# Performance work log

Measured on AMD Instinct MI355X. Metric: run time of the kernel, lower is better.

## Reference

```python
import jax, jax.numpy as jnp
import numpy as np

B, C, D, H = 2, 1024, 1024, 16
DH = D // H
EPS = 1e-8


def setup_inputs() -> dict:
    key = jax.random.key(0)
    ks = jax.random.split(key, 12)
    s = 0.02
    return {
        "x": jax.random.normal(ks[0], (B, C, D), dtype=jnp.float32),
        "rms_w": jnp.ones((C, D), dtype=jnp.float32),
        "rms_b": jnp.zeros((C, D), dtype=jnp.float32),
        "Wqkv": jax.random.normal(ks[1], (3 * D, D), dtype=jnp.float32) * s,
        "Wout": jax.random.normal(ks[2], (D, D), dtype=jnp.float32) * s,
        "bout": jnp.zeros((D,), dtype=jnp.float32),
        "Wf": jax.random.normal(ks[3], (D, D), dtype=jnp.float32) * s,
        "bf": jnp.zeros((D,), dtype=jnp.float32),
        "Ww": jax.random.normal(ks[4], (D, D), dtype=jnp.float32) * s,
        "bw": jnp.zeros((D,), dtype=jnp.float32),
        "Wv": jax.random.normal(ks[5], (D, D), dtype=jnp.float32) * s,
        "bv": jnp.zeros((D,), dtype=jnp.float32),
        "beta": jnp.ones((1,), dtype=jnp.float32),
    }


def _rope_cos_sin(C, dh):
    # faithful to source: theta = 10000 ** (-2*(i-1)/dh), i in [0, dh//2)
    i = jnp.arange(dh // 2, dtype=jnp.float32)
    theta = 10000.0 ** (-2.0 * (i - 1.0) / dh)            # [dh//2]
    ang = jnp.arange(C, dtype=jnp.float32)[:, None] * theta  # [C, dh//2]
    return jnp.cos(ang), jnp.sin(ang)


def _rotate(t, cos, sin):
    # equivalent to einsum('bhci,cij->bhcj', t, R) with the source R
    ev, od = t[..., 0::2], t[..., 1::2]          # [B,H,C,dh//2]
    out_ev = ev * cos + od * sin
    out_od = -ev * sin + od * cos
    return jnp.stack([out_ev, out_od], axis=-1).reshape(t.shape)


def _rmsnorm(x, w, b):
    rms = jnp.sqrt(jnp.mean(x * x, axis=-1, keepdims=True) + EPS)
    return w * (x / rms) + b


def _attention(x, Wqkv, Wout, bout):
    qkv = x @ Wqkv.T                               # [B,C,3D]
    q, k, v = jnp.split(qkv, 3, axis=-1)
    def heads(t):
        return t.reshape(B, C, H, DH).transpose(0, 2, 1, 3)  # [B,H,C,dh]
    q, k, v = heads(q), heads(k), heads(v)
    cos, sin = _rope_cos_sin(C, DH)
    qr = _rotate(q, cos, sin)
    kr = _rotate(k, cos, sin)
    scale = 1.0 / jnp.sqrt(jnp.float32(DH))
    num = jnp.exp(jnp.einsum('bhid,bhjd->bhij', qr, kr) * scale)
    den = jnp.sum(jnp.exp(jnp.einsum('bhid,bhjd->bhij', q, k) * scale),
                  axis=-1, keepdims=True)
    attn = num / den
    mask = jnp.tril(jnp.ones((C, C), dtype=bool))
    attn = jnp.where(mask[None, None], attn, 0.0)
    y = attn @ v                                   # [B,H,C,dh]
    y = y.transpose(0, 2, 1, 3).reshape(B, C, D)
    return y @ Wout.T + bout


def _ffn(x, Wf, bf, Ww, bw, Wv, bv, beta):
    h = x @ Wf.T + bf
    wx = h @ Ww.T + bw
    swish = wx * jax.nn.sigmoid(beta * wx)
    return swish * (h @ Wv.T + bv)


def reference(x, rms_w, rms_b, Wqkv, Wout, bout, Wf, bf, Ww, bw, Wv, bv, beta):
    # dropout p is identity in eval mode
    x = _rmsnorm(x, rms_w, rms_b)
    x = x + _attention(x, Wqkv, Wout, bout)
    x = _rmsnorm(x, rms_w, rms_b)   # same shared RMSNorm module applied twice
    x = x + _ffn(x, Wf, bf, Ww, bw, Wv, bv, beta)
    return x
```

## Files before the change

### kernel.cpp

```cpp
#include <hip/hip_runtime.h>
#include <math.h>

#define B_ 2
#define C_ 1024
#define D_ 1024
#define H_ 16
#define DH_ 64
#define EPSF 1e-8f
#define BK 32

typedef __bf16 bf16;
typedef __attribute__((ext_vector_type(4))) __bf16 bf16x4;
typedef __attribute__((ext_vector_type(8))) __bf16 bf16x8;
typedef __attribute__((ext_vector_type(4))) float f32x4;

__device__ inline f32x4 mfma16(bf16x8 a, bf16x8 b, f32x4 c) {
  return __builtin_amdgcn_mfma_f32_16x16x32_bf16(a, b, c, 0, 0, 0);
}

__device__ inline void async16(const bf16* g, bf16* l) {
  __builtin_amdgcn_global_load_lds((const __attribute__((address_space(1))) void*)g,
                                   (__attribute__((address_space(3))) void*)l, 16, 0, 0);
}

__device__ inline float rope_theta(float i) {
  return exp2f(-13.287712379549449f * (2.0f * (i - 1.0f) * (1.0f / 64.0f)));
}

__global__ __launch_bounds__(256) void cvt_rms_kernel(const float* __restrict__ wqkv,
                                                      const float* __restrict__ wout,
                                                      const float* __restrict__ wf,
                                                      const float* __restrict__ www,
                                                      const float* __restrict__ wv,
                                                      bf16* __restrict__ wdst,
                                                      const float* __restrict__ x,
                                                      const float* __restrict__ rw,
                                                      const float* __restrict__ rb,
                                                      bf16* __restrict__ xout) {
  __shared__ float red[4];
  int t = threadIdx.x;
  if (blockIdx.x < 7 * 1024) {
    int seg = blockIdx.x >> 10;
    int local = (blockIdx.x & 1023) * 1024 + t * 4;
    const float* src = seg < 3 ? wqkv + (size_t)seg * (D_ * D_)
                     : seg == 3 ? wout : seg == 4 ? wf : seg == 5 ? www : wv;
    float4 v = *(const float4*)(src + local);
    bf16x4 o;
    o[0] = (bf16)v.x; o[1] = (bf16)v.y; o[2] = (bf16)v.z; o[3] = (bf16)v.w;
    *(bf16x4*)(wdst + (size_t)seg * (D_ * D_) + local) = o;
    return;
  }
  int row = blockIdx.x - 7 * 1024;
  int c = row & (C_ - 1);
  float4 xv = *(const float4*)(x + (size_t)row * D_ + t * 4);
  float ss = xv.x * xv.x + xv.y * xv.y + xv.z * xv.z + xv.w * xv.w;
#pragma unroll
  for (int m = 1; m < 64; m <<= 1) ss += __shfl_xor(ss, m, 64);
  if ((t & 63) == 0) red[t >> 6] = ss;
  __syncthreads();
  float tot = red[0] + red[1] + red[2] + red[3];
  float inv = rsqrtf(tot * (1.0f / D_) + EPSF);
  float4 wv4 = *(const float4*)(rw + (size_t)c * D_ + t * 4);
  float4 bv4 = *(const float4*)(rb + (size_t)c * D_ + t * 4);
  bf16x4 ov;
  ov[0] = (bf16)(wv4.x * (xv.x * inv) + bv4.x);
  ov[1] = (bf16)(wv4.y * (xv.y * inv) + bv4.y);
  ov[2] = (bf16)(wv4.z * (xv.z * inv) + bv4.z);
  ov[3] = (bf16)(wv4.w * (xv.w * inv) + bv4.w);
  *(bf16x4*)(xout + (size_t)row * D_ + t * 4) = ov;
}

__global__ __launch_bounds__(256) void rmsnorm_bf16_kernel(const bf16* __restrict__ x,
                                                           const float* __restrict__ w,
                                                           const float* __restrict__ b,
                                                           bf16* __restrict__ out) {
  int row = blockIdx.x;
  int c = row & (C_ - 1);
  int t = threadIdx.x;
  bf16x4 xv = *(const bf16x4*)(x + (size_t)row * D_ + t * 4);
  float f0 = (float)xv[0], f1 = (float)xv[1], f2 = (float)xv[2], f3 = (float)xv[3];
  float ss = f0 * f0 + f1 * f1 + f2 * f2 + f3 * f3;
#pragma unroll
  for (int m = 1; m < 64; m <<= 1) ss += __shfl_xor(ss, m, 64);
  __shared__ float red[4];
  if ((t & 63) == 0) red[t >> 6] = ss;
  __syncthreads();
  float tot = red[0] + red[1] + red[2] + red[3];
  float inv = rsqrtf(tot * (1.0f / D_) + EPSF);
  float4 wv = *(const float4*)(w + (size_t)c * D_ + t * 4);
  float4 bv = *(const float4*)(b + (size_t)c * D_ + t * 4);
  bf16x4 ov;
  ov[0] = (bf16)(wv.x * (f0 * inv) + bv.x);
  ov[1] = (bf16)(wv.y * (f1 * inv) + bv.y);
  ov[2] = (bf16)(wv.z * (f2 * inv) + bv.z);
  ov[3] = (bf16)(wv.w * (f3 * inv) + bv.w);
  *(bf16x4*)(out + (size_t)row * D_ + t * 4) = ov;
}

template <int BMt, int BNt>
__global__ __launch_bounds__(256) void gemm_lds(const bf16* __restrict__ A,
                                                const bf16* __restrict__ W,
                                                const float* __restrict__ bias,
                                                const bf16* __restrict__ R,
                                                bf16* __restrict__ Cout,
                                                int M, int N, int K) {
  constexpr int MT = BMt / 32;
  constexpr int NT = BNt / 32;
  __shared__ bf16 sa[BMt * BK];
  __shared__ bf16 sb[BNt * BK];
  int t = threadIdx.x, l = t & 63, w = t >> 6;
  int m0 = blockIdx.y * BMt;
  int n0 = blockIdx.x * BNt;
  int wm = (w >> 1) * (BMt / 2), wn = (w & 1) * (BNt / 2);
  int lm = l & 15, lq = l >> 4;
  f32x4 acc[MT][NT] = {};

  for (int k0 = 0; k0 < K; k0 += BK) {
    __syncthreads();
#pragma unroll
    for (int p = 0; p < BMt / 64; ++p) {
      int lin = p * 256 + t;
      async16(A + (size_t)(m0 + (lin >> 2)) * K + k0 + (lin & 3) * 8, sa + lin * 8);
    }
#pragma unroll
    for (int p = 0; p < BNt / 64; ++p) {
      int lin = p * 256 + t;
      async16(W + (size_t)(n0 + (lin >> 2)) * K + k0 + (lin & 3) * 8, sb + lin * 8);
    }
    __syncthreads();
    bf16x8 af[MT], bfr[NT];
#pragma unroll
    for (int mt = 0; mt < MT; ++mt)
      af[mt] = *(const bf16x8*)(sa + (wm + mt * 16 + lm) * BK + lq * 8);
#pragma unroll
    for (int nt = 0; nt < NT; ++nt)
      bfr[nt] = *(const bf16x8*)(sb + (wn + nt * 16 + lm) * BK + lq * 8);
#pragma unroll
    for (int mt = 0; mt < MT; ++mt)
#pragma unroll
      for (int nt = 0; nt < NT; ++nt)
        acc[mt][nt] = mfma16(af[mt], bfr[nt], acc[mt][nt]);
  }
#pragma unroll
  for (int mt = 0; mt < MT; ++mt)
#pragma unroll
    for (int nt = 0; nt < NT; ++nt) {
      int col = n0 + wn + nt * 16 + lm;
      float bb = bias ? bias[col] : 0.0f;
#pragma unroll
      for (int r = 0; r < 4; ++r) {
        int row = m0 + wm + mt * 16 + lq * 4 + r;
        float v = acc[mt][nt][r] + bb;
        if (R) v += (float)R[(size_t)row * N + col];
        Cout[(size_t)row * N + col] = (bf16)v;
      }
    }
}

__global__ __launch_bounds__(256) void gemm_qkv_kernel(const bf16* __restrict__ A,
                                                       const bf16* __restrict__ W,
                                                       bf16* __restrict__ qkv,
                                                       bf16* __restrict__ vt) {
  constexpr int BMt = 128, BNt = 64, MT = 4, NT = 2;
  const int N = 3 * D_, K = D_;
  __shared__ bf16 sa[BMt * BK];
  __shared__ bf16 sb[BNt * BK];
  __shared__ bf16 tv[64 * 136];
  int t = threadIdx.x, l = t & 63, w = t >> 6;
  int m0 = blockIdx.y * BMt;
  int n0 = blockIdx.x * BNt;
  int wm = (w >> 1) * 64, wn = (w & 1) * 32;
  int lm = l & 15, lq = l >> 4;
  f32x4 acc[MT][NT] = {};

  for (int k0 = 0; k0 < K; k0 += BK) {
    __syncthreads();
#pragma unroll
    for (int p = 0; p < 2; ++p) {
      int lin = p * 256 + t;
      async16(A + (size_t)(m0 + (lin >> 2)) * K + k0 + (lin & 3) * 8, sa + lin * 8);
    }
    async16(W + (size_t)(n0 + (t >> 2)) * K + k0 + (t & 3) * 8, sb + t * 8);
    __syncthreads();
    bf16x8 af[MT], bfr[NT];
#pragma unroll
    for (int mt = 0; mt < MT; ++mt)
      af[mt] = *(const bf16x8*)(sa + (wm + mt * 16 + lm) * BK + lq * 8);
#pragma unroll
    for (int nt = 0; nt < NT; ++nt)
      bfr[nt] = *(const bf16x8*)(sb + (wn + nt * 16 + lm) * BK + lq * 8);
#pragma unroll
    for (int mt = 0; mt < MT; ++mt)
#pragma unroll
      for (int nt = 0; nt < NT; ++nt)
        acc[mt][nt] = mfma16(af[mt], bfr[nt], acc[mt][nt]);
  }
  if (n0 < 2 * D_) {
#pragma unroll
    for (int mt = 0; mt < MT; ++mt)
#pragma unroll
      for (int nt = 0; nt < NT; ++nt) {
        int col = n0 + wn + nt * 16 + lm;
#pragma unroll
        for (int r = 0; r < 4; ++r) {
          int row = m0 + wm + mt * 16 + lq * 4 + r;
          qkv[(size_t)row * N + col] = (bf16)acc[mt][nt][r];
        }
      }
  } else {
#pragma unroll
    for (int mt = 0; mt < MT; ++mt)
#pragma unroll
      for (int nt = 0; nt < NT; ++nt) {
        int dh = wn + nt * 16 + lm;
#pragma unroll
        for (int r = 0; r < 4; ++r)
          tv[dh * 136 + wm + mt * 16 + lq * 4 + r] = (bf16)acc[mt][nt][r];
      }
    __syncthreads();
    int h = (n0 - 2 * D_) >> 6;
    int bb = m0 >> 10;
    int mloc = m0 & 1023;
    size_t vbase = (size_t)((bb * H_ + h) * DH_) * C_;
#pragma unroll
    for (int p = 0; p < 4; ++p) {
      int lin = p * 256 + t;
      int dh = lin >> 4;
      int mm = (lin & 15) * 8;
      *(int4*)(vt + vbase + (size_t)dh * C_ + mloc + mm) = *(int4*)(tv + dh * 136 + mm);
    }
  }
}

__global__ __launch_bounds__(256) void gemm_ffn_kernel(const bf16* __restrict__ A,
                                                       const bf16* __restrict__ Ww,
                                                       const bf16* __restrict__ Wv,
                                                       const float* __restrict__ bw,
                                                       const float* __restrict__ bv,
                                                       const bf16* __restrict__ x3,
                                                       const float* __restrict__ beta_p,
                                                       float* __restrict__ out) {
  __shared__ bf16 sa[64 * BK];
  __shared__ bf16 sb1[64 * BK];
  __shared__ bf16 sb2[64 * BK];
  int t = threadIdx.x, l = t & 63, w = t >> 6;
  int m0 = blockIdx.y * 64, n0 = blockIdx.x * 64;
  int wm = (w >> 1) * 32, wn = (w & 1) * 32;
  int lm = l & 15, lq = l >> 4;
  float beta = beta_p[0];
  f32x4 acc1[2][2] = {}, acc2[2][2] = {};

  for (int k0 = 0; k0 < D_; k0 += BK) {
    __syncthreads();
    async16(A + (size_t)(m0 + (t >> 2)) * D_ + k0 + (t & 3) * 8, sa + t * 8);
    async16(Ww + (size_t)(n0 + (t >> 2)) * D_ + k0 + (t & 3) * 8, sb1 + t * 8);
    async16(Wv + (size_t)(n0 + (t >> 2)) * D_ + k0 + (t & 3) * 8, sb2 + t * 8);
    __syncthreads();
    bf16x8 af[2], b1f[2], b2f[2];
#pragma unroll
    for (int mt = 0; mt < 2; ++mt)
      af[mt] = *(const bf16x8*)(sa + (wm + mt * 16 + lm) * BK + lq * 8);
#pragma unroll
    for (int nt = 0; nt < 2; ++nt) {
      b1f[nt] = *(const bf16x8*)(sb1 + (wn + nt * 16 + lm) * BK + lq * 8);
      b2f[nt] = *(const bf16x8*)(sb2 + (wn + nt * 16 + lm) * BK + lq * 8);
    }
#pragma unroll
    for (int mt = 0; mt < 2; ++mt)
#pragma unroll
      for (int nt = 0; nt < 2; ++nt) {
        acc1[mt][nt] = mfma16(af[mt], b1f[nt], acc1[mt][nt]);
        acc2[mt][nt] = mfma16(af[mt], b2f[nt], acc2[mt][nt]);
      }
  }
#pragma unroll
  for (int mt = 0; mt < 2; ++mt)
#pragma unroll
    for (int nt = 0; nt < 2; ++nt) {
      int col = n0 + wn + nt * 16 + lm;
      float bbw = bw[col], bbv = bv[col];
#pragma unroll
      for (int r = 0; r < 4; ++r) {
        int row = m0 + wm + mt * 16 + lq * 4 + r;
        float z = acc1[mt][nt][r] + bbw;
        float g = acc2[mt][nt][r] + bbv;
        float sw = z / (1.0f + __expf(-beta * z));
        out[(size_t)row * D_ + col] = (float)x3[(size_t)row * D_ + col] + sw * g;
      }
    }
}

__global__ __launch_bounds__(256) void attn_kernel(const bf16* __restrict__ qkv,
                                                   const bf16* __restrict__ vt,
                                                   float* __restrict__ yp,
                                                   float* __restrict__ dp) {
  __shared__ bf16 sk[64 * 72];
  __shared__ bf16 skr[64 * 72];
  __shared__ bf16 sv[64 * 72];
  __shared__ bf16 pl[4][16 * 72];
  int t = threadIdx.x, l = t & 63, w = t >> 6;
  int blk = blockIdx.x;
  int it = blk >> 6;
  int r6 = blk & 63;
  int b = r6 >> 5;
  int h = (r6 >> 1) & 15;
  int half = r6 & 1;
  int i_base = it * 64 + w * 16;
  int lm = l & 15, lq = l >> 4;
  const float scale = 0.125f;
  int jf = half << 9;

  size_t hq = (size_t)h * DH_;
  size_t qrow = (size_t)(b * C_ + i_base + lm) * (3 * D_) + hq;
  bf16x8 qp[2], qrf[2];
  float cq = (float)(i_base + lm);
#pragma unroll
  for (int kk = 0; kk < 2; ++kk) {
    qp[kk] = *(const bf16x8*)(qkv + qrow + kk * 32 + lq * 8);
#pragma unroll
    for (int j = 0; j < 4; ++j) {
      float ip = (float)(kk * 16 + lq * 4 + j);
      float ang = cq * rope_theta(ip);
      float sv_, cv_;
      __sincosf(ang, &sv_, &cv_);
      float qe = (float)qp[kk][2 * j], qo = (float)qp[kk][2 * j + 1];
      qrf[kk][2 * j] = (bf16)(qe * cv_ + qo * sv_);
      qrf[kk][2 * j + 1] = (bf16)(qo * cv_ - qe * sv_);
    }
  }

  float den[4] = {0.f, 0.f, 0.f, 0.f};
  f32x4 yacc[4] = {};
  int i_max = i_base + 15;
  size_t kbase = (size_t)(b * C_) * (3 * D_) + D_ + hq;
  size_t vtbase = (size_t)((b * H_ + h) * DH_) * C_;
  int sr = t >> 3;
  int sc = (t & 7) * 8;
  float th0 = rope_theta((float)((sc >> 1) + 0));
  float th1 = rope_theta((float)((sc >> 1) + 1));
  float th2 = rope_theta((float)((sc >> 1) + 2));
  float th3 = rope_theta((float)((sc >> 1) + 3));

  float cA0, sA0, cA1, sA1, cA2, sA2, cA3, sA3;
  float cB0, sB0, cB1, sB1, cB2, sB2, cB3, sB3;
  float C0, S0, C1, S1, C2, S2, C3, S3;
#define INITP(P)                                              \
  {                                                           \
    float a;                                                  \
    a = (float)(jf + sr) * th##P;                             \
    __sincosf(a, &sA##P, &cA##P);                             \
    a = (float)(jf + 32 + sr) * th##P;                        \
    __sincosf(a, &sB##P, &cB##P);                             \
    a = 64.0f * th##P;                                        \
    __sincosf(a, &S##P, &C##P);                               \
  }
  INITP(0) INITP(1) INITP(2) INITP(3)
#undef INITP

  int4 pk0, pk1, pv0, pv1;
#define FETCH_TILE(J0)                                                          \
  pk0 = *(const int4*)(qkv + kbase + (size_t)((J0) + sr) * (3 * D_) + sc);      \
  pk1 = *(const int4*)(qkv + kbase + (size_t)((J0) + 32 + sr) * (3 * D_) + sc); \
  pv0 = *(const int4*)(vt + vtbase + (size_t)sr * C_ + (J0) + sc);              \
  pv1 = *(const int4*)(vt + vtbase + (size_t)(32 + sr) * C_ + (J0) + sc);

  FETCH_TILE(jf)

  for (int j0 = jf; j0 < jf + 512; j0 += 64) {
    __syncthreads();
    *(int4*)(sk + sr * 72 + sc) = pk0;
    *(int4*)(sk + (32 + sr) * 72 + sc) = pk1;
    *(int4*)(sv + sr * 72 + sc) = pv0;
    *(int4*)(sv + (32 + sr) * 72 + sc) = pv1;
    {
      bf16x8 k0 = *(bf16x8*)&pk0, k1 = *(bf16x8*)&pk1;
      bf16x8 r0, r1;
#define ROT2(KV, RV, CC, SS, J)                           \
  {                                                       \
    float e = (float)KV[2 * J], o = (float)KV[2 * J + 1]; \
    RV[2 * J] = (bf16)(e * CC + o * SS);                  \
    RV[2 * J + 1] = (bf16)(o * CC - e * SS);              \
  }
      ROT2(k0, r0, cA0, sA0, 0) ROT2(k0, r0, cA1, sA1, 1)
      ROT2(k0, r0, cA2, sA2, 2) ROT2(k0, r0, cA3, sA3, 3)
      ROT2(k1, r1, cB0, sB0, 0) ROT2(k1, r1, cB1, sB1, 1)
      ROT2(k1, r1, cB2, sB2, 2) ROT2(k1, r1, cB3, sB3, 3)
#undef ROT2
#define STEP(CX, SX, P)                 \
  {                                     \
    float nc = CX * C##P - SX * S##P;   \
    SX = SX * C##P + CX * S##P;         \
    CX = nc;                            \
  }
      STEP(cA0, sA0, 0) STEP(cA1, sA1, 1) STEP(cA2, sA2, 2) STEP(cA3, sA3, 3)
      STEP(cB0, sB0, 0) STEP(cB1, sB1, 1) STEP(cB2, sB2, 2) STEP(cB3, sB3, 3)
#undef STEP
      *(int4*)(skr + sr * 72 + sc) = *(int4*)&r0;
      *(int4*)(skr + (32 + sr) * 72 + sc) = *(int4*)&r1;
    }
    __syncthreads();
    if (j0 + 64 < jf + 512) {
      FETCH_TILE(j0 + 64)
    }
#pragma unroll
    for (int js = 0; js < 64; js += 16) {
      bf16x8 kf0 = *(const bf16x8*)(sk + (js + lm) * 72 + lq * 8);
      bf16x8 kf1 = *(const bf16x8*)(sk + (js + lm) * 72 + 32 + lq * 8);
      f32x4 s = {0.f, 0.f, 0.f, 0.f};
      s = mfma16(qp[0], kf0, s);
      s = mfma16(qp[1], kf1, s);
#pragma unroll
      for (int r = 0; r < 4; ++r) den[r] += __expf(s[r] * scale);
    }
    if (j0 <= i_max) {
#pragma unroll
      for (int js = 0; js < 64; js += 16) {
        bf16x8 kf0 = *(const bf16x8*)(skr + (js + lm) * 72 + lq * 8);
        bf16x8 kf1 = *(const bf16x8*)(skr + (js + lm) * 72 + 32 + lq * 8);
        f32x4 s = {0.f, 0.f, 0.f, 0.f};
        s = mfma16(qrf[0], kf0, s);
        s = mfma16(qrf[1], kf1, s);
#pragma unroll
        for (int r = 0; r < 4; ++r) {
          int jg = j0 + js + lm;
          int ig = i_base + lq * 4 + r;
          float p = (jg <= ig) ? __expf(s[r] * scale) : 0.0f;
          pl[w][(lq * 4 + r) * 72 + js + lm] = (bf16)p;
        }
      }
      __builtin_amdgcn_wave_barrier();
      bf16x8 pf0 = *(const bf16x8*)(pl[w] + lm * 72 + lq * 8);
      bf16x8 pf1 = *(const bf16x8*)(pl[w] + lm * 72 + 32 + lq * 8);
#pragma unroll
      for (int tt = 0; tt < 4; ++tt) {
        bf16x8 vf0 = *(const bf16x8*)(sv + (tt * 16 + lm) * 72 + lq * 8);
        bf16x8 vf1 = *(const bf16x8*)(sv + (tt * 16 + lm) * 72 + 32 + lq * 8);
        yacc[tt] = mfma16(pf0, vf0, mfma16(pf1, vf1, yacc[tt]));
      }
      __builtin_amdgcn_wave_barrier();
    }
  }
#undef FETCH_TILE
#pragma unroll
  for (int r = 0; r < 4; ++r) {
    float d = den[r];
    d += __shfl_xor(d, 1, 64);
    d += __shfl_xor(d, 2, 64);
    d += __shfl_xor(d, 4, 64);
    d += __shfl_xor(d, 8, 64);
    if (lm == 0) dp[(size_t)blk * 64 + w * 16 + lq * 4 + r] = d;
  }
  size_t yb = (size_t)blk * 4096;
#pragma unroll
  for (int tt = 0; tt < 4; ++tt)
#pragma unroll
    for (int r = 0; r < 4; ++r)
      yp[yb + (size_t)(w * 16 + lq * 4 + r) * 64 + tt * 16 + lm] = yacc[tt][r];
}

__global__ __launch_bounds__(256) void combine_kernel(const float* __restrict__ yp,
                                                      const float* __restrict__ dp,
                                                      bf16* __restrict__ y) {
  int cb = blockIdx.x;
  int it = cb >> 5;
  int b = (cb >> 4) & 1;
  int h = cb & 15;
  int t = threadIdx.x;
  int row = t >> 2;
  int cg = (t & 3) * 16;
  size_t p0 = (size_t)(cb * 2) * 4096 + (size_t)row * 64 + cg;
  size_t p1 = p0 + 4096;
  float inv = 1.0f / (dp[(size_t)(cb * 2) * 64 + row] + dp[(size_t)(cb * 2 + 1) * 64 + row]);
  bf16x8 o0, o1;
#pragma unroll
  for (int c = 0; c < 8; ++c) o0[c] = (bf16)((yp[p0 + c] + yp[p1 + c]) * inv);
#pragma unroll
  for (int c = 0; c < 8; ++c) o1[c] = (bf16)((yp[p0 + 8 + c] + yp[p1 + 8 + c]) * inv);
  size_t ob = (size_t)(b * C_ + it * 64 + row) * D_ + h * DH_ + cg;
  *(bf16x8*)(y + ob) = o0;
  *(bf16x8*)(y + ob + 8) = o1;
}

extern "C" void kernel_launch(void* const* d_in, const int* in_sizes, int n_in,
                              void* d_out, int out_size, void* d_ws, size_t ws_size,
                              hipStream_t stream) {
  const float* x = (const float*)d_in[0];
  const float* rms_w = (const float*)d_in[1];
  const float* rms_b = (const float*)d_in[2];
  const float* Wqkv = (const float*)d_in[3];
  const float* Wout = (const float*)d_in[4];
  const float* bout = (const float*)d_in[5];
  const float* Wf = (const float*)d_in[6];
  const float* bfp = (const float*)d_in[7];
  const float* Ww = (const float*)d_in[8];
  const float* bw = (const float*)d_in[9];
  const float* Wv = (const float*)d_in[10];
  const float* bv = (const float*)d_in[11];
  const float* beta = (const float*)d_in[12];
  float* out = (float*)d_out;

  bf16* ws = (bf16*)d_ws;
  const size_t DD = (size_t)D_ * D_;
  const size_t MC = (size_t)B_ * C_;
  bf16* wb = ws;
  bf16* x1 = ws + 7 * DD;
  bf16* qkv = ws + 9 * DD;
  bf16* vt = ws + 15 * DD;
  bf16* x2 = ws + 17 * DD;
  bf16* x3 = ws + 19 * DD;
  bf16* hbuf = ws + 21 * DD;
  float* yp = (float*)(ws + 24 * DD);
  float* dp = yp + (size_t)1024 * 4096;
  bf16* y = (bf16*)d_out;

  cvt_rms_kernel<<<7 * 1024 + MC, 256, 0, stream>>>(Wqkv, Wout, Wf, Ww, Wv, wb, x, rms_w,
                                                    rms_b, x1);
  gemm_qkv_kernel<<<dim3(3 * D_ / 64, MC / 128), 256, 0, stream>>>(x1, wb, qkv, vt);
  attn_kernel<<<B_ * H_ * 16 * 2, 256, 0, stream>>>(qkv, vt, yp, dp);
  combine_kernel<<<B_ * H_ * 16, 256, 0, stream>>>(yp, dp, y);
  gemm_lds<64, 64><<<dim3(D_ / 64, MC / 64), 256, 0, stream>>>(
      y, wb + 3 * DD, bout, x1, x2, MC, D_, D_);
  rmsnorm_bf16_kernel<<<MC, 256, 0, stream>>>(x2, rms_w, rms_b, x3);
  gemm_lds<64, 64><<<dim3(D_ / 64, MC / 64), 256, 0, stream>>>(
      x3, wb + 4 * DD, bfp, nullptr, hbuf, MC, D_, D_);
  gemm_ffn_kernel<<<dim3(D_ / 64, MC / 64), 256, 0, stream>>>(
      hbuf, wb + 5 * DD, wb + 6 * DD, bw, bv, x3, beta, out);
}
```

Before: 225.2 us.

## Double GEMM K-tile to 64 with fragment-ordered LDS layout

All three bf16 GEMM kernels now stage a 64-wide K slice per iteration instead of 32, which halves the number of barrier pairs per GEMM. The async global-to-LDS copies write data in MFMA fragment order, so each lane's 16-byte fragment read is contiguous and conflict-free. The QKV kernel aliases its V-transpose scratch onto the staging buffer to keep LDS usage flat, and adds a barrier before reusing it. Doubling the LDS tile in the FFN kernel may reduce occupancy, and the global access pattern for each staged row is now less contiguous.

```diff
diff --git a/kernel.cpp b/kernel.cpp
--- a/kernel.cpp
+++ b/kernel.cpp
@@ -7,7 +7,6 @@
 #define H_ 16
 #define DH_ 64
 #define EPSF 1e-8f
-#define BK 32
 
 typedef __bf16 bf16;
 typedef __attribute__((ext_vector_type(4))) __bf16 bf16x4;
@@ -26,6 +25,16 @@
 __device__ inline float rope_theta(float i) {
   return exp2f(-13.287712379549449f * (2.0f * (i - 1.0f) * (1.0f / 64.0f)));
 }
+
+#define STAGE(SRC, DST, ROWS, BASEROW, LDK)                                          \
+  _Pragma("unroll") for (int p = 0; p < (ROWS) / 32; ++p) {                          \
+    int lin = p * 256 + t;                                                           \
+    int rg = lin >> 7, kkh = (lin >> 6) & 1, lq2 = (lin >> 4) & 3, lm2 = lin & 15;   \
+    async16(SRC + (size_t)((BASEROW) + rg * 16 + lm2) * (LDK) + k0 + kkh * 32 +      \
+                lq2 * 8,                                                             \
+            DST + lin * 8);                                                          \
+  }
+#define FRAG(BUF, RG, KKH) (*(const bf16x8*)((BUF) + ((RG)*128 + (KKH)*64 + lq * 16 + lm) * 8))
 
 __global__ __launch_bounds__(256) void cvt_rms_kernel(const float* __restrict__ wqkv,
                                                       const float* __restrict__ wout,
@@ -106,40 +115,34 @@
                                                 int M, int N, int K) {
   constexpr int MT = BMt / 32;
   constexpr int NT = BNt / 32;
-  __shared__ bf16 sa[BMt * BK];
-  __shared__ bf16 sb[BNt * BK];
+  __shared__ bf16 sa[BMt * 64];
+  __shared__ bf16 sb[BNt * 64];
   int t = threadIdx.x, l = t & 63, w = t >> 6;
   int m0 = blockIdx.y * BMt;
   int n0 = blockIdx.x * BNt;
   int wm = (w >> 1) * (BMt / 2), wn = (w & 1) * (BNt / 2);
   int lm = l & 15, lq = l >> 4;
+  int arg = wm >> 4, brg = wn >> 4;
   f32x4 acc[MT][NT] = {};
 
-  for (int k0 = 0; k0 < K; k0 += BK) {
-    __syncthreads();
-#pragma unroll
-    for (int p = 0; p < BMt / 64; ++p) {
-      int lin = p * 256 + t;
-      async16(A + (size_t)(m0 + (lin >> 2)) * K + k0 + (lin & 3) * 8, sa + lin * 8);
-    }
-#pragma unroll
-    for (int p = 0; p < BNt / 64; ++p) {
-      int lin = p * 256 + t;
-      async16(W + (size_t)(n0 + (lin >> 2)) * K + k0 + (lin & 3) * 8, sb + lin * 8);
-    }
-    __syncthreads();
-    bf16x8 af[MT], bfr[NT];
-#pragma unroll
-    for (int mt = 0; mt < MT; ++mt)
-      af[mt] = *(const bf16x8*)(sa + (wm + mt * 16 + lm) * BK + lq * 8);
-#pragma unroll
-    for (int nt = 0; nt < NT; ++nt)
-      bfr[nt] = *(const bf16x8*)(sb + (wn + nt * 16 + lm) * BK + lq * 8);
-#pragma unroll
-    for (int mt = 0; mt < MT; ++mt)
-#pragma unroll
-      for (int nt = 0; nt < NT; ++nt)
-        acc[mt][nt] = mfma16(af[mt], bfr[nt], acc[mt][nt]);
+  for (int k0 = 0; k0 < K; k0 += 64) {
+    __syncthreads();
+    STAGE(A, sa, BMt, m0, K)
+    STAGE(W, sb, BNt, n0, K)
+    __syncthreads();
+#pragma unroll
+    for (int kkh = 0; kkh < 2; ++kkh) {
+      bf16x8 af[MT], bfr[NT];
+#pragma unroll
+      for (int mt = 0; mt < MT; ++mt) af[mt] = FRAG(sa, arg + mt, kkh);
+#pragma unroll
+      for (int nt = 0; nt < NT; ++nt) bfr[nt] = FRAG(sb, brg + nt, kkh);
+#pragma unroll
+      for (int mt = 0; mt < MT; ++mt)
+#pragma unroll
+        for (int nt = 0; nt < NT; ++nt)
+          acc[mt][nt] = mfma16(af[mt], bfr[nt], acc[mt][nt]);
+    }
   }
 #pragma unroll
   for (int mt = 0; mt < MT; ++mt)
@@ -163,37 +166,36 @@
                                                        bf16* __restrict__ vt) {
   constexpr int BMt = 128, BNt = 64, MT = 4, NT = 2;
   const int N = 3 * D_, K = D_;
-  __shared__ bf16 sa[BMt * BK];
-  __shared__ bf16 sb[BNt * BK];
-  __shared__ bf16 tv[64 * 136];
+  __shared__ bf16 smem[BMt * 64 + BNt * 64];
+  bf16* sa = smem;
+  bf16* sb = smem + BMt * 64;
+  bf16* tv = smem;
   int t = threadIdx.x, l = t & 63, w = t >> 6;
   int m0 = blockIdx.y * BMt;
   int n0 = blockIdx.x * BNt;
   int wm = (w >> 1) * 64, wn = (w & 1) * 32;
   int lm = l & 15, lq = l >> 4;
+  int arg = wm >> 4, brg = wn >> 4;
   f32x4 acc[MT][NT] = {};
 
-  for (int k0 = 0; k0 < K; k0 += BK) {
-    __syncthreads();
-#pragma unroll
-    for (int p = 0; p < 2; ++p) {
-      int lin = p * 256 + t;
-      async16(A + (size_t)(m0 + (lin >> 2)) * K + k0 + (lin & 3) * 8, sa + lin * 8);
-    }
-    async16(W + (size_t)(n0 + (t >> 2)) * K + k0 + (t & 3) * 8, sb + t * 8);
-    __syncthreads();
-    bf16x8 af[MT], bfr[NT];
-#pragma unroll
-    for (int mt = 0; mt < MT; ++mt)
-      af[mt] = *(const bf16x8*)(sa + (wm + mt * 16 + lm) * BK + lq * 8);
-#pragma unroll
-    for (int nt = 0; nt < NT; ++nt)
-      bfr[nt] = *(const bf16x8*)(sb + (wn + nt * 16 + lm) * BK + lq * 8);
-#pragma unroll
-    for (int mt = 0; mt < MT; ++mt)
-#pragma unroll
-      for (int nt = 0; nt < NT; ++nt)
-        acc[mt][nt] = mfma16(af[mt], bfr[nt], acc[mt][nt]);
+  for (int k0 = 0; k0 < K; k0 += 64) {
+    __syncthreads();
+    STAGE(A, sa, BMt, m0, K)
+    STAGE(W, sb, BNt, n0, K)
+    __syncthreads();
+#pragma unroll
+    for (int kkh = 0; kkh < 2; ++kkh) {
+      bf16x8 af[MT], bfr[NT];
+#pragma unroll
+      for (int mt = 0; mt < MT; ++mt) af[mt] = FRAG(sa, arg + mt, kkh);
+#pragma unroll
+      for (int nt = 0; nt < NT; ++nt) bfr[nt] = FRAG(sb, brg + nt, kkh);
+#pragma unroll
+      for (int mt = 0; mt < MT; ++mt)
+#pragma unroll
+        for (int nt = 0; nt < NT; ++nt)
+          acc[mt][nt] = mfma16(af[mt], bfr[nt], acc[mt][nt]);
+    }
   }
   if (n0 < 2 * D_) {
 #pragma unroll
@@ -208,6 +210,7 @@
         }
       }
   } else {
+    __syncthreads();
 #pragma unroll
     for (int mt = 0; mt < MT; ++mt)
 #pragma unroll
@@ -240,38 +243,41 @@
                                                        const bf16* __restrict__ x3,
                                                        const float* __restrict__ beta_p,
                                                        float* __restrict__ out) {
-  __shared__ bf16 sa[64 * BK];
-  __shared__ bf16 sb1[64 * BK];
-  __shared__ bf16 sb2[64 * BK];
+  __shared__ bf16 sa[64 * 64];
+  __shared__ bf16 sb1[64 * 64];
+  __shared__ bf16 sb2[64 * 64];
   int t = threadIdx.x, l = t & 63, w = t >> 6;
   int m0 = blockIdx.y * 64, n0 = blockIdx.x * 64;
   int wm = (w >> 1) * 32, wn = (w & 1) * 32;
   int lm = l & 15, lq = l >> 4;
+  int arg = wm >> 4, brg = wn >> 4;
   float beta = beta_p[0];
   f32x4 acc1[2][2] = {}, acc2[2][2] = {};
 
-  for (int k0 = 0; k0 < D_; k0 += BK) {
-    __syncthreads();
-    async16(A + (size_t)(m0 + (t >> 2)) * D_ + k0 + (t & 3) * 8, sa + t * 8);
-    async16(Ww + (size_t)(n0 + (t >> 2)) * D_ + k0 + (t & 3) * 8, sb1 + t * 8);
-    async16(Wv + (size_t)(n0 + (t >> 2)) * D_ + k0 + (t & 3) * 8, sb2 + t * 8);
-    __syncthreads();
-    bf16x8 af[2], b1f[2], b2f[2];
-#pragma unroll
-    for (int mt = 0; mt < 2; ++mt)
-      af[mt] = *(const bf16x8*)(sa + (wm + mt * 16 + lm) * BK + lq * 8);
-#pragma unroll
-    for (int nt = 0; nt < 2; ++nt) {
-      b1f[nt] = *(const bf16x8*)(sb1 + (wn + nt * 16 + lm) * BK + lq * 8);
-      b2f[nt] = *(const bf16x8*)(sb2 + (wn + nt * 16 + lm) * BK + lq * 8);
-    }
-#pragma unroll
-    for (int mt = 0; mt < 2; ++mt)
+  for (int k0 = 0; k0 < D_; k0 += 64) {
+    __syncthreads();
+    STAGE(A, sa, 64, m0, D_)
+    STAGE(Ww, sb1, 64, n0, D_)
+    STAGE(Wv, sb2, 64, n0, D_)
+    __syncthreads();
+#pragma unroll
+    for (int kkh = 0; kkh < 2; ++kkh) {
+      bf16x8 af[2], b1f[2], b2f[2];
+#pragma unroll
+      for (int mt = 0; mt < 2; ++mt) af[mt] = FRAG(sa, arg + mt, kkh);
 #pragma unroll
       for (int nt = 0; nt < 2; ++nt) {
-        acc1[mt][nt] = mfma16(af[mt], b1f[nt], acc1[mt][nt]);
-        acc2[mt][nt] = mfma16(af[mt], b2f[nt], acc2[mt][nt]);
-      }
+        b1f[nt] = FRAG(sb1, brg + nt, kkh);
+        b2f[nt] = FRAG(sb2, brg + nt, kkh);
+      }
+#pragma unroll
+      for (int mt = 0; mt < 2; ++mt)
+#pragma unroll
+        for (int nt = 0; nt < 2; ++nt) {
+          acc1[mt][nt] = mfma16(af[mt], b1f[nt], acc1[mt][nt]);
+          acc2[mt][nt] = mfma16(af[mt], b2f[nt], acc2[mt][nt]);
+        }
+    }
   }
 #pragma unroll
   for (int mt = 0; mt < 2; ++mt)
@@ -344,15 +350,15 @@
   float cA0, sA0, cA1, sA1, cA2, sA2, cA3, sA3;
   float cB0, sB0, cB1, sB1, cB2, sB2, cB3, sB3;
   float C0, S0, C1, S1, C2, S2, C3, S3;
-#define INITP(P)                                              \
-  {                                                           \
-    float a;                                                  \
-    a = (float)(jf + sr) * th##P;                             \
-    __sincosf(a, &sA##P, &cA##P);                             \
-    a = (float)(jf + 32 + sr) * th##P;                        \
-    __sincosf(a, &sB##P, &cB##P);                             \
-    a = 64.0f * th##P;                                        \
-    __sincosf(a, &S##P, &C##P);                               \
+#define INITP(P)                       \
+  {                                    \
+    float a;                           \
+    a = (float)(jf + sr) * th##P;      \
+    __sincosf(a, &sA##P, &cA##P);      \
+    a = (float)(jf + 32 + sr) * th##P; \
+    __sincosf(a, &sB##P, &cB##P);      \
+    a = 64.0f * th##P;                 \
+    __sincosf(a, &S##P, &C##P);        \
   }
   INITP(0) INITP(1) INITP(2) INITP(3)
 #undef INITP
@@ -386,11 +392,11 @@
       ROT2(k1, r1, cB0, sB0, 0) ROT2(k1, r1, cB1, sB1, 1)
       ROT2(k1, r1, cB2, sB2, 2) ROT2(k1, r1, cB3, sB3, 3)
 #undef ROT2
-#define STEP(CX, SX, P)                 \
-  {                                     \
-    float nc = CX * C##P - SX * S##P;   \
-    SX = SX * C##P + CX * S##P;         \
-    CX = nc;                            \
+#define STEP(CX, SX, P)               \
+  {                                   \
+    float nc = CX * C##P - SX * S##P; \
+    SX = SX * C##P + CX * S##P;       \
+    CX = nc;                          \
   }
       STEP(cA0, sA0, 0) STEP(cA1, sA1, 1) STEP(cA2, sA2, 2) STEP(cA3, sA3, 3)
       STEP(cB0, sB0, 0) STEP(cB1, sB1, 1) STEP(cB2, sB2, 2) STEP(cB3, sB3, 3)
```

Result: slower. 250.9 us (+11.4%).
